# Kernel tuning notes

Hardware: AMD Instinct MI355X
Metric: run time of the kernel (lower is better)

Reference implementation:

```python
import jax, jax.numpy as jnp
import numpy as np
from jax import lax

C = 512          # n_embed
M = 512          # num_memory_slots
K = 3            # conv_kernel_size
B, T = 8, 8192
EPS = 1e-5


def _layernorm(x, g, b):
    mu = jnp.mean(x, axis=-1, keepdims=True)
    var = jnp.var(x, axis=-1, keepdims=True)
    return (x - mu) * lax.rsqrt(var + EPS) * g + b


def setup_inputs() -> dict:
    key = jax.random.key(0)
    ks = jax.random.split(key, 10)
    s = 0.02
    return {
        "x": jax.random.normal(ks[0], (B, T, C), jnp.float32),
        "conv_w": jax.random.normal(ks[1], (C, 1, K), jnp.float32) * s,   # depthwise (O, I/g=1, K)
        "conv_b": jnp.zeros((C,), jnp.float32),
        "memory_bank": jax.random.normal(ks[2], (M, C), jnp.float32) * (1.0 / np.sqrt(C)),
        "gate_w": jax.random.normal(ks[3], (C, 2 * C), jnp.float32) * s,
        "gate_b": jnp.zeros((2 * C,), jnp.float32),
        "w1": jax.random.normal(ks[4], (C, 4 * C), jnp.float32) * s,
        "b1": jnp.zeros((4 * C,), jnp.float32),
        "w2": jax.random.normal(ks[5], (4 * C, C), jnp.float32) * s,
        "b2": jnp.zeros((C,), jnp.float32),
        "ln1_g": jnp.ones((C,), jnp.float32),
        "ln1_b": jnp.zeros((C,), jnp.float32),
        "ln2_g": jnp.ones((C,), jnp.float32),
        "ln2_b": jnp.zeros((C,), jnp.float32),
    }


def reference(x, conv_w, conv_b, memory_bank, gate_w, gate_b,
              w1, b1, w2, b2, ln1_g, ln1_b, ln2_g, ln2_b):
    residual = x
    x_norm = _layernorm(x, ln1_g, ln1_b)                      # (B,T,C)

    # causal depthwise conv: left-pad by K-1 (PyTorch pads both sides then slices [:T])
    xt = jnp.transpose(x_norm, (0, 2, 1))                     # (B,C,T)
    local = lax.conv_general_dilated(
        xt, conv_w, window_strides=(1,), padding=[(K - 1, 0)],
        dimension_numbers=("NCT", "OIT", "NCT"), feature_group_count=C)
    local = jnp.transpose(local + conv_b[None, :, None], (0, 2, 1))  # (B,T,C)

    # memory-bank softmax attention
    scores = jnp.einsum("btc,mc->btm", x_norm, memory_bank)   # (B,T,M)
    weights = jax.nn.softmax(scores, axis=-1)
    global_ctx = jnp.einsum("btm,mc->btc", weights, memory_bank)

    # sigmoid gating
    gates = x_norm @ gate_w + gate_b                          # (B,T,2C)
    lg, gg = gates[..., :C], gates[..., C:]
    fused = jax.nn.sigmoid(lg) * local + jax.nn.sigmoid(gg) * global_ctx

    x = residual + fused
    h = _layernorm(x, ln2_g, ln2_b)
    ffn = jax.nn.gelu(h @ w1 + b1, approximate=False) @ w2 + b2  # dropout is identity (eval)
    return x + ffn
```

## Files before the change

### kernel.cpp

```cpp
#include <hip/hip_runtime.h>
#include <math.h>

#define NTOK 65536
#define T_   8192
#define C_   512

typedef short short8 __attribute__((ext_vector_type(8)));
typedef float f32x4  __attribute__((ext_vector_type(4)));

#define GLDS(gp, lp) __builtin_amdgcn_global_load_lds( \
    (__attribute__((address_space(1))) void*)(void*)(gp), \
    (__attribute__((address_space(3))) void*)(lp), 16, 0, 0)

__device__ __forceinline__ unsigned short f2bf(float f){
  unsigned x = __float_as_uint(f);
  x += 0x7fffu + ((x >> 16) & 1u);
  return (unsigned short)(x >> 16);
}
__device__ __forceinline__ float bflo(unsigned p){ return __uint_as_float(p << 16); }
__device__ __forceinline__ float bfhi(unsigned p){ return __uint_as_float(p & 0xffff0000u); }
__device__ __forceinline__ float bfs(unsigned short u){ return __uint_as_float(((unsigned)u) << 16); }
__device__ __forceinline__ unsigned pack2(float a, float b){
  return (unsigned)f2bf(a) | ((unsigned)f2bf(b) << 16);
}
__device__ __forceinline__ int xcd_remap(int flat, int nwg){
  int q = nwg >> 3, r = nwg & 7;
  int xcd = flat & 7, idx = flat >> 3;
  return (xcd < r ? xcd * (q + 1) : r * (q + 1) + (xcd - r) * q) + idx;
}

__global__ __launch_bounds__(256) void k_prep(const float* __restrict__ mb,
                                              const float* __restrict__ gate_w,
                                              const float* __restrict__ w1,
                                              const float* __restrict__ w2,
                                              unsigned short* __restrict__ mb_bf,
                                              unsigned short* __restrict__ mbT,
                                              unsigned short* __restrict__ gwT,
                                              unsigned short* __restrict__ w1T,
                                              unsigned short* __restrict__ w2T){
  __shared__ float tile[64][65];
  const int bid = blockIdx.x;
  const float* src; unsigned short* dst; int R, S, t0;
  if (bid < 64)       { src = mb;     dst = mbT; R = 512;  S = 512;  t0 = bid; }
  else if (bid < 192) { src = gate_w; dst = gwT; R = 512;  S = 1024; t0 = bid - 64; }
  else if (bid < 448) { src = w1;     dst = w1T; R = 512;  S = 2048; t0 = bid - 192; }
  else if (bid < 704) { src = w2;     dst = w2T; R = 2048; S = 512;  t0 = bid - 448; }
  else {
    int i = (bid - 704) * 256 + threadIdx.x;
    mb_bf[i] = f2bf(mb[i]);
    return;
  }
  int ntS = S >> 6;
  int tr = t0 / ntS, ts = t0 - tr * ntS;
  int tx = threadIdx.x & 63, tg = threadIdx.x >> 6;
  #pragma unroll
  for (int rr = tg; rr < 64; rr += 4)
    tile[rr][tx] = src[(size_t)(tr * 64 + rr) * S + ts * 64 + tx];
  __syncthreads();
  #pragma unroll
  for (int rr = tg; rr < 64; rr += 4)
    dst[(size_t)(ts * 64 + rr) * R + tr * 64 + tx] = f2bf(tile[tx][rr]);
}

__global__ __launch_bounds__(256) void k_ln4(const float* __restrict__ x,
                                             const float* __restrict__ g,
                                             const float* __restrict__ b,
                                             unsigned* __restrict__ outbf){
  const int row  = blockIdx.x * 4 + (threadIdx.x >> 6);
  const int lane = threadIdx.x & 63;
  const float4* xr = (const float4*)(x + (size_t)row * C_) + lane * 2;
  float4 v0 = xr[0], v1 = xr[1];
  float s  = v0.x + v0.y + v0.z + v0.w + v1.x + v1.y + v1.z + v1.w;
  float ss = v0.x*v0.x + v0.y*v0.y + v0.z*v0.z + v0.w*v0.w
           + v1.x*v1.x + v1.y*v1.y + v1.z*v1.z + v1.w*v1.w;
  #pragma unroll
  for (int o = 32; o; o >>= 1){ s += __shfl_xor(s, o); ss += __shfl_xor(ss, o); }
  float mu  = s * (1.0f / C_);
  float var = ss * (1.0f / C_) - mu * mu;
  float rs = rsqrtf(var + 1e-5f);
  const float4* gr = (const float4*)g + lane * 2;
  const float4* br = (const float4*)b + lane * 2;
  float4 g0 = gr[0], g1 = gr[1], b0 = br[0], b1 = br[1];
  uint4 o4;
  o4.x = pack2((v0.x - mu) * rs * g0.x + b0.x, (v0.y - mu) * rs * g0.y + b0.y);
  o4.y = pack2((v0.z - mu) * rs * g0.z + b0.z, (v0.w - mu) * rs * g0.w + b0.w);
  o4.z = pack2((v1.x - mu) * rs * g1.x + b1.x, (v1.y - mu) * rs * g1.y + b1.y);
  o4.w = pack2((v1.z - mu) * rs * g1.z + b1.z, (v1.w - mu) * rs * g1.w + b1.w);
  ((uint4*)(outbf + (size_t)row * 256))[lane] = o4;
}

__global__ __launch_bounds__(256) void k_conv8(const unsigned* __restrict__ xn,
                                               const float* __restrict__ w,
                                               const float* __restrict__ bias,
                                               unsigned* __restrict__ loc,
                                               int base){
  const int cp = threadIdx.x;
  const size_t n0 = (size_t)blockIdx.x * 8 + (size_t)base;
  const int t0 = (int)(n0 & (T_ - 1));
  const int c = cp * 2;
  const float w00 = w[c*3], w01 = w[c*3+1], w02 = w[c*3+2];
  const float w10 = w[c*3+3], w11 = w[c*3+4], w12 = w[c*3+5];
  const float b0 = bias[c], b1 = bias[c+1];
  unsigned vm2 = (t0 >= 2) ? xn[(n0 - 2) * 256 + cp] : 0u;
  unsigned vm1 = (t0 >= 1) ? xn[(n0 - 1) * 256 + cp] : 0u;
  size_t obase = (n0 - (size_t)base) * 256 + cp;
  #pragma unroll
  for (int k = 0; k < 8; k++){
    unsigned v = xn[(n0 + k) * 256 + cp];
    float r0 = b0 + bflo(v)*w02 + bflo(vm1)*w01 + bflo(vm2)*w00;
    float r1 = b1 + bfhi(v)*w12 + bfhi(vm1)*w11 + bfhi(vm2)*w10;
    loc[obase + (size_t)k * 256] = pack2(r0, r1);
    vm2 = vm1; vm1 = v;
  }
}

__global__ __launch_bounds__(256) void k_softmax4(unsigned* __restrict__ sw){
  const int row  = blockIdx.x * 4 + (threadIdx.x >> 6);
  const int lane = threadIdx.x & 63;
  uint4 p = ((uint4*)(sw + (size_t)row * 256))[lane];
  float v[8];
  v[0]=bflo(p.x); v[1]=bfhi(p.x); v[2]=bflo(p.y); v[3]=bfhi(p.y);
  v[4]=bflo(p.z); v[5]=bfhi(p.z); v[6]=bflo(p.w); v[7]=bfhi(p.w);
  float mx = v[0];
  #pragma unroll
  for (int k = 1; k < 8; k++) mx = fmaxf(mx, v[k]);
  #pragma unroll
  for (int o = 32; o; o >>= 1) mx = fmaxf(mx, __shfl_xor(mx, o));
  float s = 0.f;
  #pragma unroll
  for (int k = 0; k < 8; k++){ v[k] = __expf(v[k] - mx); s += v[k]; }
  #pragma unroll
  for (int o = 32; o; o >>= 1) s += __shfl_xor(s, o);
  float inv = 1.0f / s;
  p.x = pack2(v[0]*inv, v[1]*inv); p.y = pack2(v[2]*inv, v[3]*inv);
  p.z = pack2(v[4]*inv, v[5]*inv); p.w = pack2(v[6]*inv, v[7]*inv);
  ((uint4*)(sw + (size_t)row * 256))[lane] = p;
}

#define PH_PRE  { __builtin_amdgcn_s_barrier(); \
                  asm volatile("s_waitcnt lgkmcnt(0)" ::: "memory"); \
                  __builtin_amdgcn_sched_barrier(0); }
#define PH_END  __builtin_amdgcn_s_barrier();
#define VMW2    asm volatile("s_waitcnt vmcnt(2)" ::: "memory");
#define VMW0    asm volatile("s_waitcnt vmcnt(0)" ::: "memory");

template<int EPI, int K, int N>
__global__ __launch_bounds__(512, 2) void k_g256(const unsigned short* __restrict__ A,
                                                 const unsigned short* __restrict__ Bt,
                                                 void* __restrict__ out,
                                                 const float* __restrict__ bias,
                                                 const float* __restrict__ add){
  __shared__ char smem[131072];
  const int tid  = threadIdx.x;
  const int lane = tid & 63;
  const int w    = tid >> 6;
  const int wr   = w >> 2, wc = w & 3;
  const int nwg  = gridDim.x * gridDim.y;
  const int wgid = xcd_remap(blockIdx.y * gridDim.x + blockIdx.x, nwg);
  const long bcol = (long)(wgid % gridDim.x) * 256;
  const long brow = (long)(wgid / gridDim.x) * 256;
  const int lr = lane & 15;
  const int lk = (lane >> 4) * 16;
  const int srow  = tid >> 3;
  const int sbyte = ((tid & 7) * 16) ^ ((srow & 7) << 4);
  const unsigned swb = (unsigned)(w * 1024);
  const int rsw = (lr & 7) << 4;

  f32x4 acc[8][4];
  #pragma unroll
  for (int i = 0; i < 8; i++)
    #pragma unroll
    for (int j = 0; j < 4; j++){ f32x4 z = {0.f,0.f,0.f,0.f}; acc[i][j] = z; }

  const char* Ab = (const char*)(A + brow * (long)K);
  const char* Bb = (const char*)(Bt + bcol * (long)K);

  auto ST = [&](const char* g, int ldsoff, int row0, int kt){
    GLDS(g + ((long)(row0 + srow) * K + (long)kt * 64) * 2 + sbyte,
         smem + ldsoff + row0 * 128 + swb);
  };
  auto stA0 = [&](int b, int kt){ ST(Ab, b*32768, 0,  kt); ST(Ab, b*32768, 128, kt); };
  auto stA1 = [&](int b, int kt){ ST(Ab, b*32768, 64, kt); ST(Ab, b*32768, 192, kt); };
  auto stB0 = [&](int b, int kt){ ST(Bb, 65536+b*32768, 0,   kt); ST(Bb, 65536+b*32768, 64,  kt); };
  auto stB1 = [&](int b, int kt){ ST(Bb, 65536+b*32768, 128, kt); ST(Bb, 65536+b*32768, 192, kt); };

  short8 afr[4][2], bfr[2][2];
  auto RDA = [&](int b, int qm){
    #pragma unroll
    for (int mj = 0; mj < 4; mj++)
      #pragma unroll
      for (int kk = 0; kk < 2; kk++)
        afr[mj][kk] = *(const short8*)(smem + b*32768 +
            (wr*128 + (qm*4+mj)*16 + lr) * 128 + ((kk*64 + lk) ^ rsw));
  };
  auto RDB = [&](int b, int qn){
    #pragma unroll
    for (int nj = 0; nj < 2; nj++)
      #pragma unroll
      for (int kk = 0; kk < 2; kk++)
        bfr[nj][kk] = *(const short8*)(smem + 65536 + b*32768 +
            (wc*64 + (qn*2+nj)*16 + lr) * 128 + ((kk*64 + lk) ^ rsw));
  };
  auto MM = [&](int qm, int qn){
    __builtin_amdgcn_s_setprio(1);
    #pragma unroll
    for (int mj = 0; mj < 4; mj++)
      #pragma unroll
      for (int nj = 0; nj < 2; nj++)
        #pragma unroll
        for (int kk = 0; kk < 2; kk++)
          acc[qm*4+mj][qn*2+nj] =
            __builtin_amdgcn_mfma_f32_16x16x32_bf16(afr[mj][kk], bfr[nj][kk],
                                                    acc[qm*4+mj][qn*2+nj], 0, 0, 0);
    __builtin_amdgcn_s_setprio(0);
  };

  constexpr int nt    = K >> 6;
  constexpr int niter = nt >> 1;

  stA0(0, 0); stA1(0, 0); stB0(0, 0); stB1(0, 0);
  stA0(1, 1);
  VMW2;
  __builtin_amdgcn_s_barrier();

  #pragma unroll 1
  for (int i = 0; i < niter; i++){
    const int t = 2 * i;
    RDA(0,0); RDB(0,0); stA1(1, t+1);
    PH_PRE; MM(0,0); PH_END;
    RDA(0,1); stB0(1, t+1);
    PH_PRE; MM(1,0); PH_END;
    RDA(0,0); RDB(0,1); stB1(1, t+1);
    PH_PRE; MM(0,1); PH_END;
    RDA(0,1); if (t + 2 < nt) stA0(0, t+2);
    PH_PRE; MM(1,1);
    if (t + 2 < nt) { VMW2; } else { VMW0; }
    PH_END;
    RDA(1,0); RDB(1,0); if (t + 2 < nt) stA1(0, t+2);
    PH_PRE; MM(0,0); PH_END;
    RDA(1,1); if (t + 2 < nt) stB0(0, t+2);
    PH_PRE; MM(1,0); PH_END;
    RDA(1,0); RDB(1,1); if (t + 2 < nt) stB1(0, t+2);
    PH_PRE; MM(0,1); PH_END;
    RDA(1,1); if (t + 3 < nt) stA0(1, t+3);
    PH_PRE; MM(1,1);
    if (i + 1 < niter){ if (t + 3 < nt) { VMW2; } else { VMW0; } }
    PH_END;
  }

  const long rb = brow + wr * 128;
  const long cb = bcol + wc * 64;
  #pragma unroll
  for (int mi = 0; mi < 8; mi++){
    #pragma unroll
    for (int ni = 0; ni < 4; ni++){
      long rg0 = rb + mi * 16 + (lane >> 4) * 4;
      long cg  = cb + ni * 16 + lr;
      #pragma unroll
      for (int j = 0; j < 4; j++){
        long oi = (rg0 + j) * (long)N + cg;
        float v = acc[mi][ni][j];
        if (EPI == 1){
          ((unsigned short*)out)[oi] = f2bf(v);
        } else if (EPI == 3){
          v += bias[cg];
          v = 0.5f * v * (1.0f + erff(v * 0.70710678118654752f));
          ((unsigned short*)out)[oi] = f2bf(v);
        } else {
          v += bias[cg] + add[oi];
          ((float*)out)[oi] = v;
        }
      }
    }
  }
}

__global__ __launch_bounds__(512, 2) void k_gc256(const unsigned short* __restrict__ A,
                                                  const unsigned short* __restrict__ Bt,
                                                  const float* __restrict__ gb,
                                                  const unsigned short* __restrict__ loc,
                                                  const unsigned short* __restrict__ ctx,
                                                  const float* __restrict__ x,
                                                  float* __restrict__ x2){
  __shared__ char smem[131072];
  const int tid  = threadIdx.x;
  const int lane = tid & 63;
  const int w    = tid >> 6;
  const int wr   = w >> 2, wc = w & 3;
  const int nwg  = gridDim.x * gridDim.y;
  const int wgid = xcd_remap(blockIdx.y * gridDim.x + blockIdx.x, nwg);
  const int  bcol = (wgid % gridDim.x) * 128;
  const long brow = (long)(wgid / gridDim.x) * 256;
  const int K = 512;
  const int lr = lane & 15;
  const int lk = (lane >> 4) * 16;
  const int srow  = tid >> 3;
  const int sbyte = ((tid & 7) * 16) ^ ((srow & 7) << 4);
  const unsigned swb = (unsigned)(w * 1024);
  const int rsw = (lr & 7) << 4;

  f32x4 acc[8][2][2];
  #pragma unroll
  for (int i = 0; i < 8; i++)
    #pragma unroll
    for (int j = 0; j < 2; j++)
      #pragma unroll
      for (int h = 0; h < 2; h++){ f32x4 z = {0.f,0.f,0.f,0.f}; acc[i][j][h] = z; }

  const char* Ab  = (const char*)(A + brow * (long)K);
  const char* BbL = (const char*)(Bt + (long)bcol * K);
  const char* BbG = (const char*)(Bt + (long)(512 + bcol) * K);

  auto ST = [&](const char* g, int ldsoff, int row0, int kt){
    GLDS(g + ((long)(row0 + srow) * K + (long)kt * 64) * 2 + sbyte,
         smem + ldsoff + row0 * 128 + swb);
  };
  auto stA0 = [&](int b, int kt){ ST(Ab, b*32768, 0,  kt); ST(Ab, b*32768, 128, kt); };
  auto stA1 = [&](int b, int kt){ ST(Ab, b*32768, 64, kt); ST(Ab, b*32768, 192, kt); };
  auto stBL = [&](int b, int kt){ ST(BbL, 65536+b*32768,       0, kt); ST(BbL, 65536+b*32768,       64, kt); };
  auto stBG = [&](int b, int kt){ ST(BbG, 65536+b*32768+16384, 0, kt); ST(BbG, 65536+b*32768+16384, 64, kt); };

  short8 afr[4][2], bfr[2][2];
  auto RDA = [&](int b, int qm){
    #pragma unroll
    for (int mj = 0; mj < 4; mj++)
      #pragma unroll
      for (int kk = 0; kk < 2; kk++)
        afr[mj][kk] = *(const short8*)(smem + b*32768 +
            (wr*128 + (qm*4+mj)*16 + lr) * 128 + ((kk*64 + lk) ^ rsw));
  };
  auto RDB = [&](int b, int h){
    #pragma unroll
    for (int nj = 0; nj < 2; nj++)
      #pragma unroll
      for (int kk = 0; kk < 2; kk++)
        bfr[nj][kk] = *(const short8*)(smem + 65536 + b*32768 + h*16384 +
            (wc*32 + nj*16 + lr) * 128 + ((kk*64 + lk) ^ rsw));
  };
  auto MM = [&](int qm, int h){
    __builtin_amdgcn_s_setprio(1);
    #pragma unroll
    for (int mj = 0; mj < 4; mj++)
      #pragma unroll
      for (int nj = 0; nj < 2; nj++)
        #pragma unroll
        for (int kk = 0; kk < 2; kk++)
          acc[qm*4+mj][nj][h] =
            __builtin_amdgcn_mfma_f32_16x16x32_bf16(afr[mj][kk], bfr[nj][kk],
                                                    acc[qm*4+mj][nj][h], 0, 0, 0);
    __builtin_amdgcn_s_setprio(0);
  };

  constexpr int nt = 8, niter = 4;

  stA0(0, 0); stA1(0, 0); stBL(0, 0); stBG(0, 0);
  stA0(1, 1);
  VMW2;
  __builtin_amdgcn_s_barrier();

  #pragma unroll 1
  for (int i = 0; i < niter; i++){
    const int t = 2 * i;
    RDA(0,0); RDB(0,0); stA1(1, t+1);
    PH_PRE; MM(0,0); PH_END;
    RDA(0,1); stBL(1, t+1);
    PH_PRE; MM(1,0); PH_END;
    RDA(0,0); RDB(0,1); stBG(1, t+1);
    PH_PRE; MM(0,1); PH_END;
    RDA(0,1); if (t + 2 < nt) stA0(0, t+2);
    PH_PRE; MM(1,1);
    if (t + 2 < nt) { VMW2; } else { VMW0; }
    PH_END;
    RDA(1,0); RDB(1,0); if (t + 2 < nt) stA1(0, t+2);
    PH_PRE; MM(0,0); PH_END;
    RDA(1,1); if (t + 2 < nt) stBL(0, t+2);
    PH_PRE; MM(1,0); PH_END;
    RDA(1,0); RDB(1,1); if (t + 2 < nt) stBG(0, t+2);
    PH_PRE; MM(0,1); PH_END;
    RDA(1,1); if (t + 3 < nt) stA0(1, t+3);
    PH_PRE; MM(1,1);
    if (i + 1 < niter){ if (t + 3 < nt) { VMW2; } else { VMW0; } }
    PH_END;
  }

  const long rbase = brow + wr * 128;
  const int  cb_   = bcol + wc * 32;
  #pragma unroll
  for (int mi = 0; mi < 8; mi++){
    #pragma unroll
    for (int ni = 0; ni < 2; ni++){
      long rg0 = rbase + mi * 16 + (lane >> 4) * 4;
      int  cg  = cb_ + ni * 16 + lr;
      float bL = gb[cg], bG = gb[512 + cg];
      #pragma unroll
      for (int j = 0; j < 4; j++){
        long rg = rg0 + j;
        long oi = rg * 512 + cg;
        float vL = 1.0f / (1.0f + __expf(-(acc[mi][ni][0][j] + bL)));
        float vG = 1.0f / (1.0f + __expf(-(acc[mi][ni][1][j] + bG)));
        x2[oi] = x[oi] + vL * bfs(loc[oi]) + vG * bfs(ctx[oi]);
      }
    }
  }
}

extern "C" void kernel_launch(void* const* d_in, const int* in_sizes, int n_in,
                              void* d_out, int out_size, void* d_ws, size_t ws_size,
                              hipStream_t stream){
  const float* x      = (const float*)d_in[0];
  const float* conv_w = (const float*)d_in[1];
  const float* conv_b = (const float*)d_in[2];
  const float* mb     = (const float*)d_in[3];
  const float* gate_w = (const float*)d_in[4];
  const float* gate_b = (const float*)d_in[5];
  const float* w1     = (const float*)d_in[6];
  const float* b1     = (const float*)d_in[7];
  const float* w2     = (const float*)d_in[8];
  const float* b2     = (const float*)d_in[9];
  const float* ln1g   = (const float*)d_in[10];
  const float* ln1b   = (const float*)d_in[11];
  const float* ln2g   = (const float*)d_in[12];
  const float* ln2b   = (const float*)d_in[13];

  char* ws = (char*)d_ws;
  const size_t MB = 1024ull * 1024ull;
  unsigned short* mb_bf = (unsigned short*)(ws + 0);
  unsigned short* mbT   = (unsigned short*)(ws + 512 * 1024);
  unsigned short* gwT   = (unsigned short*)(ws + 1 * MB);
  unsigned short* w1T   = (unsigned short*)(ws + 2 * MB);
  unsigned short* w2T   = (unsigned short*)(ws + 4 * MB);
  unsigned short* xn    = (unsigned short*)(ws + 8 * MB);
  char* region = ws + 72 * MB;

  int S;
  if      (ws_size >= 264 * MB) S = 65536;
  else if (ws_size >= 120 * MB) S = 16384;
  else                          S = 4096;
  const int S2 = S / 2;
  const int NC  = NTOK / S;
  const int NC2 = NTOK / S2;

  unsigned short* loc_c = (unsigned short*)(region);
  unsigned short* ctx_c = (unsigned short*)(region + (size_t)S * 1024);
  unsigned short* sco_c = (unsigned short*)(region + (size_t)S * 2048);
  unsigned short* f1    = (unsigned short*)(region);

  k_prep<<<1728, 256, 0, stream>>>(mb, gate_w, w1, w2, mb_bf, mbT, gwT, w1T, w2T);

  k_ln4<<<NTOK / 4, 256, 0, stream>>>(x, ln1g, ln1b, (unsigned*)xn);

  for (int c = 0; c < NC; c++){
    const int base = c * S;
    const unsigned short* xnc = xn + (size_t)base * 512;
    k_conv8<<<S / 8, 256, 0, stream>>>((const unsigned*)xn, conv_w, conv_b,
                                       (unsigned*)loc_c, base);
    k_g256<1, 512, 512><<<dim3(2, S / 256), 512, 0, stream>>>(xnc, mb_bf, sco_c,
                                                              nullptr, nullptr);
    k_softmax4<<<S / 4, 256, 0, stream>>>((unsigned*)sco_c);
    k_g256<1, 512, 512><<<dim3(2, S / 256), 512, 0, stream>>>(sco_c, mbT, ctx_c,
                                                              nullptr, nullptr);
    k_gc256<<<dim3(4, S / 256), 512, 0, stream>>>(xnc, gwT, gate_b,
                                                  loc_c, ctx_c,
                                                  x + (size_t)base * 512,
                                                  (float*)d_out + (size_t)base * 512);
  }

  k_ln4<<<NTOK / 4, 256, 0, stream>>>((const float*)d_out, ln2g, ln2b, (unsigned*)xn);

  for (int c = 0; c < NC2; c++){
    const int base = c * S2;
    k_g256<3, 512, 2048><<<dim3(8, S2 / 256), 512, 0, stream>>>(xn + (size_t)base * 512,
                                                                w1T, f1, b1, nullptr);
    k_g256<4, 2048, 512><<<dim3(2, S2 / 256), 512, 0, stream>>>(f1, w2T,
                                                                (float*)d_out + (size_t)base * 512,
                                                                b2,
                                                                (const float*)d_out + (size_t)base * 512);
  }
}
```

Before: 784.8 us.

## Process multiple M-tiles per workgroup with continuous cross-tile K pipeline

Result: slower. 1.088 ms (+38.7%).

```diff
diff --git a/kernel.cpp b/kernel.cpp
--- a/kernel.cpp
+++ b/kernel.cpp
@@ -144,7 +144,7 @@
 #define VMW2    asm volatile("s_waitcnt vmcnt(2)" ::: "memory");
 #define VMW0    asm volatile("s_waitcnt vmcnt(0)" ::: "memory");
 
-template<int EPI, int K, int N>
+template<int EPI, int K, int N, int MPER>
 __global__ __launch_bounds__(512, 2) void k_g256(const unsigned short* __restrict__ A,
                                                  const unsigned short* __restrict__ Bt,
                                                  void* __restrict__ out,
@@ -157,8 +157,8 @@
   const int wr   = w >> 2, wc = w & 3;
   const int nwg  = gridDim.x * gridDim.y;
   const int wgid = xcd_remap(blockIdx.y * gridDim.x + blockIdx.x, nwg);
-  const long bcol = (long)(wgid % gridDim.x) * 256;
-  const long brow = (long)(wgid / gridDim.x) * 256;
+  const long bcol  = (long)(wgid % gridDim.x) * 256;
+  const long brow0 = (long)(wgid / gridDim.x) * (256 * MPER);
   const int lr = lane & 15;
   const int lk = (lane >> 4) * 16;
   const int srow  = tid >> 3;
@@ -172,17 +172,29 @@
     #pragma unroll
     for (int j = 0; j < 4; j++){ f32x4 z = {0.f,0.f,0.f,0.f}; acc[i][j] = z; }
 
-  const char* Ab = (const char*)(A + brow * (long)K);
+  const char* Ab = (const char*)(A + brow0 * (long)K);
   const char* Bb = (const char*)(Bt + bcol * (long)K);
+
+  constexpr int nt    = K >> 6;
+  constexpr int gtot  = nt * MPER;
+  constexpr int niter = gtot >> 1;
 
   auto ST = [&](const char* g, int ldsoff, int row0, int kt){
     GLDS(g + ((long)(row0 + srow) * K + (long)kt * 64) * 2 + sbyte,
          smem + ldsoff + row0 * 128 + swb);
   };
-  auto stA0 = [&](int b, int kt){ ST(Ab, b*32768, 0,  kt); ST(Ab, b*32768, 128, kt); };
-  auto stA1 = [&](int b, int kt){ ST(Ab, b*32768, 64, kt); ST(Ab, b*32768, 192, kt); };
-  auto stB0 = [&](int b, int kt){ ST(Bb, 65536+b*32768, 0,   kt); ST(Bb, 65536+b*32768, 64,  kt); };
-  auto stB1 = [&](int b, int kt){ ST(Bb, 65536+b*32768, 128, kt); ST(Bb, 65536+b*32768, 192, kt); };
+  auto stA0 = [&](int b, int gt){
+    const char* Am = Ab + (long)(gt / nt) * 256 * K * 2; int kt = gt % nt;
+    ST(Am, b*32768, 0,  kt); ST(Am, b*32768, 128, kt);
+  };
+  auto stA1 = [&](int b, int gt){
+    const char* Am = Ab + (long)(gt / nt) * 256 * K * 2; int kt = gt % nt;
+    ST(Am, b*32768, 64, kt); ST(Am, b*32768, 192, kt);
+  };
+  auto stB0 = [&](int b, int gt){ int kt = gt % nt;
+    ST(Bb, 65536+b*32768, 0,   kt); ST(Bb, 65536+b*32768, 64,  kt); };
+  auto stB1 = [&](int b, int gt){ int kt = gt % nt;
+    ST(Bb, 65536+b*32768, 128, kt); ST(Bb, 65536+b*32768, 192, kt); };
 
   short8 afr[4][2], bfr[2][2];
   auto RDA = [&](int b, int qm){
@@ -214,9 +226,37 @@
                                                     acc[qm*4+mj][qn*2+nj], 0, 0, 0);
     __builtin_amdgcn_s_setprio(0);
   };
-
-  constexpr int nt    = K >> 6;
-  constexpr int niter = nt >> 1;
+  auto EPIL = [&](int m){
+    const long rb = brow0 + (long)m * 256 + wr * 128;
+    const long cb = bcol + wc * 64;
+    #pragma unroll
+    for (int mi = 0; mi < 8; mi++){
+      #pragma unroll
+      for (int ni = 0; ni < 4; ni++){
+        long rg0 = rb + mi * 16 + (lane >> 4) * 4;
+        long cg  = cb + ni * 16 + lr;
+        #pragma unroll
+        for (int j = 0; j < 4; j++){
+          long oi = (rg0 + j) * (long)N + cg;
+          float v = acc[mi][ni][j];
+          if (EPI == 1){
+            ((unsigned short*)out)[oi] = f2bf(v);
+          } else if (EPI == 3){
+            v += bias[cg];
+            v = 0.5f * v * (1.0f + erff(v * 0.70710678118654752f));
+            ((unsigned short*)out)[oi] = f2bf(v);
+          } else {
+            v += bias[cg] + add[oi];
+            ((float*)out)[oi] = v;
+          }
+        }
+      }
+    }
+    #pragma unroll
+    for (int ii = 0; ii < 8; ii++)
+      #pragma unroll
+      for (int jj = 0; jj < 4; jj++){ f32x4 z = {0.f,0.f,0.f,0.f}; acc[ii][jj] = z; }
+  };
 
   stA0(0, 0); stA1(0, 0); stB0(0, 0); stB1(0, 0);
   stA0(1, 1);
@@ -232,49 +272,25 @@
     PH_PRE; MM(1,0); PH_END;
     RDA(0,0); RDB(0,1); stB1(1, t+1);
     PH_PRE; MM(0,1); PH_END;
-    RDA(0,1); if (t + 2 < nt) stA0(0, t+2);
+    RDA(0,1); if (t + 2 < gtot) stA0(0, t+2);
     PH_PRE; MM(1,1);
-    if (t + 2 < nt) { VMW2; } else { VMW0; }
+    if (t + 2 < gtot) { VMW2; } else { VMW0; }
     PH_END;
-    RDA(1,0); RDB(1,0); if (t + 2 < nt) stA1(0, t+2);
+    RDA(1,0); RDB(1,0); if (t + 2 < gtot) stA1(0, t+2);
     PH_PRE; MM(0,0); PH_END;
-    RDA(1,1); if (t + 2 < nt) stB0(0, t+2);
+    RDA(1,1); if (t + 2 < gtot) stB0(0, t+2);
     PH_PRE; MM(1,0); PH_END;
-    RDA(1,0); RDB(1,1); if (t + 2 < nt) stB1(0, t+2);
+    RDA(1,0); RDB(1,1); if (t + 2 < gtot) stB1(0, t+2);
     PH_PRE; MM(0,1); PH_END;
-    RDA(1,1); if (t + 3 < nt) stA0(1, t+3);
+    RDA(1,1); if (t + 3 < gtot) stA0(1, t+3);
     PH_PRE; MM(1,1);
-    if (i + 1 < niter){ if (t + 3 < nt) { VMW2; } else { VMW0; } }
+    if (i + 1 < niter){ if (t + 3 < gtot) { VMW2; } else { VMW0; } }
     PH_END;
+    if (((t + 2) % nt) == 0) EPIL((t + 1) / nt);
   }
-
-  const long rb = brow + wr * 128;
-  const long cb = bcol + wc * 64;
-  #pragma unroll
-  for (int mi = 0; mi < 8; mi++){
-    #pragma unroll
-    for (int ni = 0; ni < 4; ni++){
-      long rg0 = rb + mi * 16 + (lane >> 4) * 4;
-      long cg  = cb + ni * 16 + lr;
-      #pragma unroll
-      for (int j = 0; j < 4; j++){
-        long oi = (rg0 + j) * (long)N + cg;
-        float v = acc[mi][ni][j];
-        if (EPI == 1){
-          ((unsigned short*)out)[oi] = f2bf(v);
-        } else if (EPI == 3){
-          v += bias[cg];
-          v = 0.5f * v * (1.0f + erff(v * 0.70710678118654752f));
-          ((unsigned short*)out)[oi] = f2bf(v);
-        } else {
-          v += bias[cg] + add[oi];
-          ((float*)out)[oi] = v;
-        }
-      }
-    }
-  }
-}
-
+}
+
+template<int MPER>
 __global__ __launch_bounds__(512, 2) void k_gc256(const unsigned short* __restrict__ A,
                                                   const unsigned short* __restrict__ Bt,
                                                   const float* __restrict__ gb,
@@ -289,8 +305,8 @@
   const int wr   = w >> 2, wc = w & 3;
   const int nwg  = gridDim.x * gridDim.y;
   const int wgid = xcd_remap(blockIdx.y * gridDim.x + blockIdx.x, nwg);
-  const int  bcol = (wgid % gridDim.x) * 128;
-  const long brow = (long)(wgid / gridDim.x) * 256;
+  const int  bcol  = (wgid % gridDim.x) * 128;
+  const long brow0 = (long)(wgid / gridDim.x) * (256 * MPER);
   const int K = 512;
   const int lr = lane & 15;
   const int lk = (lane >> 4) * 16;
@@ -307,18 +323,30 @@
       #pragma unroll
       for (int h = 0; h < 2; h++){ f32x4 z = {0.f,0.f,0.f,0.f}; acc[i][j][h] = z; }
 
-  const char* Ab  = (const char*)(A + brow * (long)K);
+  const char* Ab  = (const char*)(A + brow0 * (long)K);
   const char* BbL = (const char*)(Bt + (long)bcol * K);
   const char* BbG = (const char*)(Bt + (long)(512 + bcol) * K);
+
+  constexpr int nt = 8;
+  constexpr int gtot  = nt * MPER;
+  constexpr int niter = gtot >> 1;
 
   auto ST = [&](const char* g, int ldsoff, int row0, int kt){
     GLDS(g + ((long)(row0 + srow) * K + (long)kt * 64) * 2 + sbyte,
          smem + ldsoff + row0 * 128 + swb);
   };
-  auto stA0 = [&](int b, int kt){ ST(Ab, b*32768, 0,  kt); ST(Ab, b*32768, 128, kt); };
-  auto stA1 = [&](int b, int kt){ ST(Ab, b*32768, 64, kt); ST(Ab, b*32768, 192, kt); };
-  auto stBL = [&](int b, int kt){ ST(BbL, 65536+b*32768,       0, kt); ST(BbL, 65536+b*32768,       64, kt); };
-  auto stBG = [&](int b, int kt){ ST(BbG, 65536+b*32768+16384, 0, kt); ST(BbG, 65536+b*32768+16384, 64, kt); };
+  auto stA0 = [&](int b, int gt){
+    const char* Am = Ab + (long)(gt / nt) * 256 * K * 2; int kt = gt % nt;
+    ST(Am, b*32768, 0,  kt); ST(Am, b*32768, 128, kt);
+  };
+  auto stA1 = [&](int b, int gt){
+    const char* Am = Ab + (long)(gt / nt) * 256 * K * 2; int kt = gt % nt;
+    ST(Am, b*32768, 64, kt); ST(Am, b*32768, 192, kt);
+  };
+  auto stBL = [&](int b, int gt){ int kt = gt % nt;
+    ST(BbL, 65536+b*32768,       0, kt); ST(BbL, 65536+b*32768,       64, kt); };
+  auto stBG = [&](int b, int gt){ int kt = gt % nt;
+    ST(BbG, 65536+b*32768+16384, 0, kt); ST(BbG, 65536+b*32768+16384, 64, kt); };
 
   short8 afr[4][2], bfr[2][2];
   auto RDA = [&](int b, int qm){
@@ -350,8 +378,33 @@
                                                     acc[qm*4+mj][nj][h], 0, 0, 0);
     __builtin_amdgcn_s_setprio(0);
   };
-
-  constexpr int nt = 8, niter = 4;
+  auto EPIL = [&](int m){
+    const long rbase = brow0 + (long)m * 256 + wr * 128;
+    const int  cb_   = bcol + wc * 32;
+    #pragma unroll
+    for (int mi = 0; mi < 8; mi++){
+      #pragma unroll
+      for (int ni = 0; ni < 2; ni++){
+        long rg0 = rbase + mi * 16 + (lane >> 4) * 4;
+        int  cg  = cb_ + ni * 16 + lr;
+        float bL = gb[cg], bG = gb[512 + cg];
+        #pragma unroll
+        for (int j = 0; j < 4; j++){
+          long rg = rg0 + j;
+          long oi = rg * 512 + cg;
+          float vL = 1.0f / (1.0f + __expf(-(acc[mi][ni][0][j] + bL)));
+          float vG = 1.0f / (1.0f + __expf(-(acc[mi][ni][1][j] + bG)));
+          x2[oi] = x[oi] + vL * bfs(loc[oi]) + vG * bfs(ctx[oi]);
+        }
+      }
+    }
+    #pragma unroll
+    for (int ii = 0; ii < 8; ii++)
+      #pragma unroll
+      for (int jj = 0; jj < 2; jj++)
+        #pragma unroll
+        for (int hh = 0; hh < 2; hh++){ f32x4 z = {0.f,0.f,0.f,0.f}; acc[ii][jj][hh] = z; }
+  };
 
   stA0(0, 0); stA1(0, 0); stBL(0, 0); stBG(0, 0);
   stA0(1, 1);
@@ -367,40 +420,21 @@
     PH_PRE; MM(1,0); PH_END;
     RDA(0,0); RDB(0,1); stBG(1, t+1);
     PH_PRE; MM(0,1); PH_END;
-    RDA(0,1); if (t + 2 < nt) stA0(0, t+2);
+    RDA(0,1); if (t + 2 < gtot) stA0(0, t+2);
     PH_PRE; MM(1,1);
-    if (t + 2 < nt) { VMW2; } else { VMW0; }
+    if (t + 2 < gtot) { VMW2; } else { VMW0; }
     PH_END;
-    RDA(1,0); RDB(1,0); if (t + 2 < nt) stA1(0, t+2);
+    RDA(1,0); RDB(1,0); if (t + 2 < gtot) stA1(0, t+2);
     PH_PRE; MM(0,0); PH_END;
-    RDA(1,1); if (t + 2 < nt) stBL(0, t+2);
+    RDA(1,1); if (t + 2 < gtot) stBL(0, t+2);
     PH_PRE; MM(1,0); PH_END;
-    RDA(1,0); RDB(1,1); if (t + 2 < nt) stBG(0, t+2);
+    RDA(1,0); RDB(1,1); if (t + 2 < gtot) stBG(0, t+2);
     PH_PRE; MM(0,1); PH_END;
-    RDA(1,1); if (t + 3 < nt) stA0(1, t+3);
+    RDA(1,1); if (t + 3 < gtot) stA0(1, t+3);
     PH_PRE; MM(1,1);
-    if (i + 1 < niter){ if (t + 3 < nt) { VMW2; } else { VMW0; } }
+    if (i + 1 < niter){ if (t + 3 < gtot) { VMW2; } else { VMW0; } }
     PH_END;
-  }
-
-  const long rbase = brow + wr * 128;
-  const int  cb_   = bcol + wc * 32;
-  #pragma unroll
-  for (int mi = 0; mi < 8; mi++){
-    #pragma unroll
-    for (int ni = 0; ni < 2; ni++){
-      long rg0 = rbase + mi * 16 + (lane >> 4) * 4;
-      int  cg  = cb_ + ni * 16 + lr;
-      float bL = gb[cg], bG = gb[512 + cg];
-      #pragma unroll
-      for (int j = 0; j < 4; j++){
-        long rg = rg0 + j;
-        long oi = rg * 512 + cg;
-        float vL = 1.0f / (1.0f + __expf(-(acc[mi][ni][0][j] + bL)));
-        float vG = 1.0f / (1.0f + __expf(-(acc[mi][ni][1][j] + bG)));
-        x2[oi] = x[oi] + vL * bfs(loc[oi]) + vG * bfs(ctx[oi]);
-      }
-    }
+    if (((t + 2) % nt) == 0) EPIL((t + 1) / nt);
   }
 }
 
@@ -454,26 +488,26 @@
     const unsigned short* xnc = xn + (size_t)base * 512;
     k_conv8<<<S / 8, 256, 0, stream>>>((const unsigned*)xn, conv_w, conv_b,
                                        (unsigned*)loc_c, base);
-    k_g256<1, 512, 512><<<dim3(2, S / 256), 512, 0, stream>>>(xnc, mb_bf, sco_c,
-                                                              nullptr, nullptr);
+    k_g256<1, 512, 512, 2><<<dim3(2, S / 512), 512, 0, stream>>>(xnc, mb_bf, sco_c,
+                                                                 nullptr, nullptr);
     k_softmax4<<<S / 4, 256, 0, stream>>>((unsigned*)sco_c);
-    k_g256<1, 512, 512><<<dim3(2, S / 256), 512, 0, stream>>>(sco_c, mbT, ctx_c,
-                                                              nullptr, nullptr);
-    k_gc256<<<dim3(4, S / 256), 512, 0, stream>>>(xnc, gwT, gate_b,
-                                                  loc_c, ctx_c,
-                                                  x + (size_t)base * 512,
-                                                  (float*)d_out + (size_t)base * 512);
+    k_g256<1, 512, 512, 2><<<dim3(2, S / 512), 512, 0, stream>>>(sco_c, mbT, ctx_c,
+                                                                 nullptr, nullptr);
+    k_gc256<4><<<dim3(4, S / 1024), 512, 0, stream>>>(xnc, gwT, gate_b,
+                                                      loc_c, ctx_c,
+                                                      x + (size_t)base * 512,
+                                                      (float*)d_out + (size_t)base * 512);
   }
 
   k_ln4<<<NTOK / 4, 256, 0, stream>>>((const float*)d_out, ln2g, ln2b, (unsigned*)xn);
 
   for (int c = 0; c < NC2; c++){
     const int base = c * S2;
-    k_g256<3, 512, 2048><<<dim3(8, S2 / 256), 512, 0, stream>>>(xn + (size_t)base * 512,
-                                                                w1T, f1, b1, nullptr);
-    k_g256<4, 2048, 512><<<dim3(2, S2 / 256), 512, 0, stream>>>(f1, w2T,
-                                                                (float*)d_out + (size_t)base * 512,
-                                                                b2,
-                                                                (const float*)d_out + (size_t)base * 512);
+    k_g256<3, 512, 2048, 4><<<dim3(8, S2 / 1024), 512, 0, stream>>>(xn + (size_t)base * 512,
+                                                                    w1T, f1, b1, nullptr);
+    k_g256<4, 2048, 512, 1><<<dim3(2, S2 / 256), 512, 0, stream>>>(f1, w2T,
+                                                                   (float*)d_out + (size_t)base * 512,
+                                                                   b2,
+                                                                   (const float*)d_out + (size_t)base * 512);
   }
 }
```
